# Kernel optimization log

Hardware: AMD Instinct MI355X
Metric: run time of the kernel (lower is better)

The kernel has to match this reference:

```python
import jax, jax.numpy as jnp
import numpy as np

N = 100000   # nodes
E = 1600000  # edges
IN = 3       # in_channels
H = 32       # hidden_channels
C = 10       # num_classes_dynamic (== num output classes here)
G = 64       # number of graphs in the batch


def setup_inputs() -> dict:
    key = jax.random.key(0)
    ks = jax.random.split(key, 12)
    def w(k, shape, fan_in):
        return jax.random.normal(k, shape, jnp.float32) / np.sqrt(fan_in).astype(np.float32)
    inp = {}
    inp["x"] = jax.random.normal(ks[0], (N, IN), jnp.float32)
    inp["edge_index"] = jax.random.randint(ks[1], (2, E), 0, N, jnp.int32)
    inp["batch"] = jnp.sort(jax.random.randint(ks[2], (N,), 0, G, jnp.int32))
    # per-class linear filters (DynamicEdgeConv.filters)
    inp["filt_W"] = w(ks[3], (C, IN, H), IN)
    inp["filt_b"] = jnp.zeros((C, H), jnp.float32)
    # shared edge MLP: Linear(2H,H) -> ReLU -> Linear(H,H)
    inp["mlp_W1"] = w(ks[4], (2 * H, H), 2 * H)
    inp["mlp_b1"] = jnp.zeros((H,), jnp.float32)
    inp["mlp_W2"] = w(ks[5], (H, H), H)
    inp["mlp_b2"] = jnp.zeros((H,), jnp.float32)
    # GCN layers (gcn1 input dim hardcoded 323 = IN + C*H)
    inp["gcn1_W"] = w(ks[6], (IN + C * H, H), IN + C * H)
    inp["gcn1_b"] = jnp.zeros((H,), jnp.float32)
    inp["gcn2_W"] = w(ks[7], (H, H), H)
    inp["gcn2_b"] = jnp.zeros((H,), jnp.float32)
    # classifier
    inp["cls_W"] = w(ks[8], (H, C), H)
    inp["cls_b"] = jnp.zeros((C,), jnp.float32)
    return inp


def _gcn_conv(x, W, b, row, col, dinv):
    # PyG GCNConv: add self-loops, sym-normalize, aggregate src->dst
    xw = x @ W                                   # [N, H]
    norm = dinv[row] * dinv[col]                 # [E]
    out = jax.ops.segment_sum(xw[row] * norm[:, None], col, num_segments=x.shape[0])
    out = out + xw * (dinv * dinv)[:, None]      # self-loop term, norm = 1/deg_i
    return out + b


def _forward(x, edge_index, batch, filt_W, filt_b, mlp_W1, mlp_b1, mlp_W2, mlp_b2,
             gcn1_W, gcn1_b, gcn2_W, gcn2_b, cls_W, cls_b):
    row, col = edge_index[0], edge_index[1]
    n = x.shape[0]

    # DynamicEdgeConv: per-class filter -> gather(row,col) -> edge MLP -> scatter_add into col
    def per_class(_, wb):
        Wc, bc = wb
        xc = x @ Wc + bc                                      # [N, H]
        ef = jnp.concatenate([xc[row], xc[col]], axis=1)      # [E, 2H]
        h = jax.nn.relu(ef @ mlp_W1 + mlp_b1) @ mlp_W2 + mlp_b2
        return None, jax.ops.segment_sum(h, col, num_segments=n)
    _, aggs = jax.lax.scan(per_class, None, (filt_W, filt_b))  # [C, N, H]

    feat = jnp.concatenate([x, aggs.transpose(1, 0, 2).reshape(n, -1)], axis=1)  # [N, IN + C*H]

    deg = jax.ops.segment_sum(jnp.ones(row.shape[0], x.dtype), col, num_segments=n) + 1.0
    dinv = deg ** -0.5
    h1 = jax.nn.relu(_gcn_conv(feat, gcn1_W, gcn1_b, row, col, dinv))
    h2 = jax.nn.relu(_gcn_conv(h1, gcn2_W, gcn2_b, row, col, dinv))

    counts = jax.ops.segment_sum(jnp.ones(n, x.dtype), batch, num_segments=G)
    pooled = jax.ops.segment_sum(h2, batch, num_segments=G) / jnp.maximum(counts, 1.0)[:, None]
    return pooled @ cls_W + cls_b                             # [G, C]


def reference(x, edge_index, batch, filt_W, filt_b, mlp_W1, mlp_b1, mlp_W2, mlp_b2,
              gcn1_W, gcn1_b, gcn2_W, gcn2_b, cls_W, cls_b):
    return _forward(x, edge_index, batch, filt_W, filt_b, mlp_W1, mlp_b1, mlp_W2, mlp_b2,
                    gcn1_W, gcn1_b, gcn2_W, gcn2_b, cls_W, cls_b)
```

## Files before the change

kernel.cpp:

```cpp
#include <hip/hip_runtime.h>

#define NN 100000
#define NE 1600000
#define HH 32
#define CC 10
#define GG 64
#define NB 391
#define PBLK 160
#define ECH 10000
#define MTOT (NB * PBLK)
#define MSB ((MTOT + 255) / 256)

typedef _Float16 half8 __attribute__((ext_vector_type(8)));
typedef _Float16 half2v __attribute__((ext_vector_type(2)));
typedef float f32x4 __attribute__((ext_vector_type(4)));

__device__ __forceinline__ half2v bch(int v) { return __builtin_bit_cast(half2v, v); }


__global__ void precompute_small(const float* __restrict__ fW, const float* __restrict__ fb,
                                 const float* __restrict__ W1, const float* __restrict__ b1,
                                 const float* __restrict__ W2, const float* __restrict__ b2,
                                 const float* __restrict__ g1W, float* __restrict__ tab,
                                 _Float16* __restrict__ Mfrag) {
    int c = blockIdx.x;
    int k = threadIdx.x >> 5;
    int j = threadIdx.x & 31;
    float m = 0.f;
    for (int mm = 0; mm < 32; ++mm)
        m += W2[k * 32 + mm] * g1W[(3 + 32 * c + mm) * 32 + j];
    tab[2240 + c * 1024 + k * 32 + j] = m;

    if (k < 3) {
        float a = 0.f, b = 0.f;
        for (int i = 0; i < 32; ++i) {
            float w = fW[c * 96 + k * 32 + i];
            a += w * W1[i * 32 + j];
            b += w * W1[(32 + i) * 32 + j];
        }
        tab[c * 96 + k * 32 + j] = a;
        tab[960 + c * 96 + k * 32 + j] = b;
    } else if (k == 3) {
        float h = b1[j];
        for (int i = 0; i < 32; ++i)
            h += fb[c * 32 + i] * (W1[i * 32 + j] + W1[(32 + i) * 32 + j]);
        tab[1920 + c * 32 + j] = h;
    } else if (k == 4 && c == 0) {
        float t = 0.f;
        for (int cc2 = 0; cc2 < CC; ++cc2)
            for (int mm = 0; mm < 32; ++mm)
                t += b2[mm] * g1W[(3 + 32 * cc2 + mm) * 32 + j];
        tab[12480 + j] = t;
    }
    __syncthreads();
    {
        int jch = k;
        int jcol = j;
        float v = tab[2240 + c * 1024 + jch * 32 + jcol];
        int knew = (c >> 1) * 64 + 2 * jch + (c & 1);
        int kc = knew >> 5, within = knew & 31;
        int jt = jcol >> 4;
        int lq = within >> 3, ii = within & 7;
        int lidx = lq * 16 + (jcol & 15);
        int flat = ((kc * 2 + jt) * 64 + lidx) * 8 + ii;
        Mfrag[flat] = (_Float16)v;
    }
}

__global__ void bucket_hist(const int* __restrict__ ei, int* __restrict__ mat) {
    __shared__ int h[NB];
    int blk = blockIdx.x, tid = threadIdx.x;
    for (int i = tid; i < NB; i += 256) h[i] = 0;
    __syncthreads();
    int base = blk * ECH;
    for (int k = tid; k < ECH; k += 256)
        atomicAdd(&h[ei[NE + base + k] >> 8], 1);
    __syncthreads();
    for (int i = tid; i < NB; i += 256) mat[i * PBLK + blk] = h[i];
}

__global__ void scan_m1(const int* __restrict__ mat, int* __restrict__ msum) {
    __shared__ int sh[256];
    int b = blockIdx.x, t = threadIdx.x;
    int i = b * 256 + t;
    sh[t] = (i < MTOT) ? mat[i] : 0;
    __syncthreads();
    for (int off = 128; off > 0; off >>= 1) {
        if (t < off) sh[t] += sh[t + off];
        __syncthreads();
    }
    if (t == 0) msum[b] = sh[0];
}

__global__ void scan_m2(int* __restrict__ msum, float* __restrict__ pooled) {
    for (int i = threadIdx.x; i < GG * 33; i += 256) pooled[i] = 0.0f;
    __shared__ int sh[256];
    int t = threadIdx.x;
    int v = (t < MSB) ? msum[t] : 0;
    sh[t] = v;
    __syncthreads();
    for (int off = 1; off < 256; off <<= 1) {
        int add = (t >= off) ? sh[t - off] : 0;
        __syncthreads();
        sh[t] += add;
        __syncthreads();
    }
    if (t < MSB) msum[t] = sh[t] - v;
}

__global__ void scan_m3(int* __restrict__ mat, const int* __restrict__ msum) {
    __shared__ int sh[256];
    int b = blockIdx.x, t = threadIdx.x;
    int i = b * 256 + t;
    int v = (i < MTOT) ? mat[i] : 0;
    sh[t] = v;
    __syncthreads();
    for (int off = 1; off < 256; off <<= 1) {
        int add = (t >= off) ? sh[t - off] : 0;
        __syncthreads();
        sh[t] += add;
        __syncthreads();
    }
    if (i < MTOT) mat[i] = sh[t] - v + msum[b];
}

__global__ void bucket_scatter(const int* __restrict__ ei, const int* __restrict__ mat,
                               unsigned int* __restrict__ part) {
    __shared__ int bas[NB];
    __shared__ int cur[NB];
    int blk = blockIdx.x, tid = threadIdx.x;
    for (int i = tid; i < NB; i += 256) { bas[i] = mat[i * PBLK + blk]; cur[i] = 0; }
    __syncthreads();
    int base = blk * ECH;
    for (int k = tid; k < ECH; k += 256) {
        int e = base + k;
        int r = ei[e];
        int c = ei[NE + e];
        int b = c >> 8;
        int local = atomicAdd(&cur[b], 1);
        part[bas[b] + local] = (unsigned)r | ((unsigned)(c & 255) << 24);
    }
}

__global__ void bucket_build(const unsigned int* __restrict__ part, const int* __restrict__ mat,
                             const float* __restrict__ x, int* __restrict__ csr_row,
                             int* __restrict__ ideg, int* __restrict__ offs,
                             float* __restrict__ dinv, float4* __restrict__ xpad,
                             uint4* __restrict__ xs) {
    __shared__ int lh[256];
    __shared__ int lex[256];
    __shared__ int cur[256];
    int b = blockIdx.x, tid = threadIdx.x;
    int ebase = mat[b * PBLK];
    int eend = (b == NB - 1) ? NE : mat[(b + 1) * PBLK];
    int m = eend - ebase;
    lh[tid] = 0;
    __syncthreads();
    for (int k = tid; k < m; k += 256) {
        unsigned v = part[ebase + k];
        atomicAdd(&lh[v >> 24], 1);
    }
    __syncthreads();
    int cnt = lh[tid];
    lex[tid] = cnt;
    __syncthreads();
    for (int off = 1; off < 256; off <<= 1) {
        int v = (tid >= off) ? lex[tid - off] : 0;
        __syncthreads();
        lex[tid] += v;
        __syncthreads();
    }
    int excl = lex[tid] - cnt;
    lex[tid] = excl;
    cur[tid] = 0;
    int n = b * 256 + tid;
    if (n < NN) {
        ideg[n] = cnt;
        offs[n] = ebase + excl;
        float di = rsqrtf((float)cnt + 1.0f);
        dinv[n] = di;
        float x0 = x[n * 3], x1 = x[n * 3 + 1], x2 = x[n * 3 + 2];
        xpad[n] = make_float4(x0, x1, x2, di);
        _Float16 hx = (_Float16)x0, hy = (_Float16)x1, hz = (_Float16)x2;
        half2v sx = {hx, hx}, sy = {hy, hy}, sz = {hz, hz};
        xs[n] = make_uint4(__builtin_bit_cast(unsigned int, sx),
                           __builtin_bit_cast(unsigned int, sy),
                           __builtin_bit_cast(unsigned int, sz), 0u);
    }
    if (b == 0 && tid == 0) offs[NN] = NE;
    __syncthreads();
    for (int k = tid; k < m; k += 256) {
        unsigned v = part[ebase + k];
        int cl = (int)(v >> 24);
        int r = (int)(v & 0x00FFFFFFu);
        int local = atomicAdd(&cur[cl], 1);
        csr_row[ebase + lex[cl] + local] = r;
    }
}

#define EC_PAIR(QQ, SRC) do { \
    half2v px_ = bch(__shfl((int)(QQ).x, (SRC), 64)); \
    half2v py_ = bch(__shfl((int)(QQ).y, (SRC), 64)); \
    half2v pz_ = bch(__shfl((int)(QQ).z, (SRC), 64)); \
    _Pragma("unroll") \
    for (int p = 0; p < 5; ++p) { \
        half2v v = va[p] + px_ * A0[p] + py_ * A1[p] + pz_ * A2[p]; \
        v = __builtin_elementwise_max(v, zero); \
        acc[p] += v; \
    } } while (0)

#define EC_FLUSH() do { \
    _Pragma("unroll") \
    for (int p = 0; p < 5; ++p) { \
        accf[2 * p]     += (float)acc[p].x; \
        accf[2 * p + 1] += (float)acc[p].y; \
        acc[p] = zero; \
    } } while (0)

#define EC_CHUNK_FROM(T0, QQ, C2) do { \
    int tfull_ = (C2) >> 1; \
    int t_ = (T0); \
    for (; t_ + 4 <= tfull_; t_ += 4) { \
        _Pragma("unroll") \
        for (int u = 0; u < 4; ++u) EC_PAIR(QQ, 2 * (t_ + u) + half); \
        EC_FLUSH(); \
    } \
    for (; t_ < tfull_; ++t_) EC_PAIR(QQ, 2 * t_ + half); \
    if ((C2) & 1) { \
        int src_ = (C2) - 1; \
        half2v px_ = bch(__shfl((int)(QQ).x, src_, 64)); \
        half2v py_ = bch(__shfl((int)(QQ).y, src_, 64)); \
        half2v pz_ = bch(__shfl((int)(QQ).z, src_, 64)); \
        if (half == 0) { \
            _Pragma("unroll") \
            for (int p = 0; p < 5; ++p) { \
                half2v v = va[p] + px_ * A0[p] + py_ * A1[p] + pz_ * A2[p]; \
                v = __builtin_elementwise_max(v, zero); \
                acc[p] += v; \
            } \
        } \
    } \
    EC_FLUSH(); } while (0)

__global__ __launch_bounds__(256, 4) void edgeconv_fused(
    const uint4* __restrict__ xs, const int* __restrict__ offs,
    const int* __restrict__ csr_row, const float* __restrict__ tab,
    _Float16* __restrict__ aggh) {
    int lane = threadIdx.x & 63;
    int j = lane & 31;
    int half = lane >> 5;

    half2v A0[5], A1[5], A2[5], B0[5], B1[5], B2[5], hb[5];
#pragma unroll
    for (int p = 0; p < 5; ++p) {
        int c0 = 2 * p, c1 = 2 * p + 1;
        A0[p] = half2v{(_Float16)tab[c0 * 96 + j],        (_Float16)tab[c1 * 96 + j]};
        A1[p] = half2v{(_Float16)tab[c0 * 96 + 32 + j],   (_Float16)tab[c1 * 96 + 32 + j]};
        A2[p] = half2v{(_Float16)tab[c0 * 96 + 64 + j],   (_Float16)tab[c1 * 96 + 64 + j]};
        B0[p] = half2v{(_Float16)tab[960 + c0 * 96 + j],      (_Float16)tab[960 + c1 * 96 + j]};
        B1[p] = half2v{(_Float16)tab[960 + c0 * 96 + 32 + j], (_Float16)tab[960 + c1 * 96 + 32 + j]};
        B2[p] = half2v{(_Float16)tab[960 + c0 * 96 + 64 + j], (_Float16)tab[960 + c1 * 96 + 64 + j]};
        hb[p] = half2v{(_Float16)tab[1920 + c0 * 32 + j], (_Float16)tab[1920 + c1 * 32 + j]};
    }
    const half2v zero = half2v{(_Float16)0.f, (_Float16)0.f};

    int wid = blockIdx.x * 4 + (threadIdx.x >> 6);
    const int ws = gridDim.x * 4;

    int n = wid;
    if (n >= NN) return;
    int e0 = offs[n];
    int e1 = offs[n + 1];
    uint4 qn = xs[n];
    int n2 = n + ws;
    int e0n = 0, e1n = 0;
    if (n2 < NN) { e0n = offs[n2]; e1n = offs[n2 + 1]; }
    uint4 q;
    {
        int ee = e0 + lane;
        int r0 = (ee < e1) ? csr_row[ee] : 0;
        q = xs[r0];
    }

    while (true) {
        int n3 = n2 + ws;
        int e0n2 = 0, e1n2 = 0;
        if (n3 < NN) { e0n2 = offs[n3]; e1n2 = offs[n3 + 1]; }
        uint4 qn2 = make_uint4(0u, 0u, 0u, 0u);
        if (n2 < NN) qn2 = xs[n2];

        bool multi = (e1 - e0) > 64;
        int pb = multi ? (e0 + 64) : e0n;
        int pe = multi ? e1 : e1n;
        int ee2 = pb + lane;
        int rn = (ee2 < pe) ? csr_row[ee2] : 0;

        half2v pxn = bch((int)qn.x), pyn = bch((int)qn.y), pzn = bch((int)qn.z);
        half2v va[5], acc[5];
        float accf[10];
#pragma unroll
        for (int p = 0; p < 5; ++p) {
            va[p] = hb[p] + pxn * B0[p] + pyn * B1[p] + pzn * B2[p];
            acc[p] = zero;
            accf[2 * p] = 0.f;
            accf[2 * p + 1] = 0.f;
        }

        int c2 = e1 - e0;
        if (c2 > 64) c2 = 64;
        int t0 = 0;
        if ((c2 >> 1) >= 4) {
#pragma unroll
            for (int u = 0; u < 4; ++u) EC_PAIR(q, 2 * u + half);
            EC_FLUSH();
            t0 = 4;
        }
        uint4 qpre = xs[rn];
        EC_CHUNK_FROM(t0, q, c2);

        if (multi) {
            int base = e0 + 64;
            uint4 qc = qpre;
            while (true) {
                int cc = e1 - base;
                if (cc > 64) cc = 64;
                int nb = base + 64;
                bool m2 = nb < e1;
                int pb2 = m2 ? nb : e0n;
                int pe2 = m2 ? e1 : e1n;
                int ee3 = pb2 + lane;
                int rn2 = (ee3 < pe2) ? csr_row[ee3] : 0;
                uint4 qp2 = xs[rn2];
                EC_CHUNK_FROM(0, qc, cc);
                qc = qp2;
                if (!m2) break;
                base = nb;
            }
            qpre = qc;
        }

#pragma unroll
        for (int c = 0; c < 10; ++c) accf[c] += __shfl_xor(accf[c], 32, 64);
        unsigned* arow32 = (unsigned*)(aggh + (size_t)n * 320);
        half2v d0 = {(_Float16)accf[2 * half],     (_Float16)accf[2 * half + 1]};
        half2v d1 = {(_Float16)accf[4 + 2 * half], (_Float16)accf[4 + 2 * half + 1]};
        arow32[lane]      = __builtin_bit_cast(unsigned, d0);
        arow32[64 + lane] = __builtin_bit_cast(unsigned, d1);
        if (half == 0) {
            half2v d2 = {(_Float16)accf[8], (_Float16)accf[9]};
            arow32[128 + lane] = __builtin_bit_cast(unsigned, d2);
        }

        if (n2 >= NN) return;
        n = n2;
        n2 = n3;
        e0 = e0n; e1 = e1n;
        e0n = e0n2; e1n = e1n2;
        qn = qn2;
        q = qpre;
    }
}

__global__ __launch_bounds__(256) void fold_mfma(
    const _Float16* __restrict__ aggh, const _Float16* __restrict__ MfragG,
    const float4* __restrict__ xpad, const int* __restrict__ ideg,
    const float* __restrict__ tab, const float* __restrict__ g1W,
    _Float16* __restrict__ y1) {
    __shared__ _Float16 Mf[10240];
    {
        const uint4* src = (const uint4*)MfragG;
        uint4* dst = (uint4*)Mf;
        for (int i = threadIdx.x; i < 1280; i += 256) dst[i] = src[i];
    }
    __syncthreads();

    int wave = blockIdx.x * 4 + (threadIdx.x >> 6);
    int lane = threadIdx.x & 63;
    int n0 = wave * 16;
    if (n0 >= NN) return;

    int m = lane & 15, q = lane >> 4;
    int arow_n = n0 + m;
    bool rowok = arow_n < NN;
    const _Float16* arow = aggh + (size_t)arow_n * 320 + q * 8;

    const half8* mf = (const half8*)Mf;
    f32x4 acc0 = {0.f, 0.f, 0.f, 0.f};
    f32x4 acc1 = {0.f, 0.f, 0.f, 0.f};

    for (int kc = 0; kc < 10; ++kc) {
        half8 a;
        if (rowok) a = *(const half8*)(arow + kc * 32);
        else {
#pragma unroll
            for (int i = 0; i < 8; ++i) a[i] = (_Float16)0.f;
        }
        half8 b0 = mf[(kc * 2 + 0) * 64 + lane];
        half8 b1 = mf[(kc * 2 + 1) * 64 + lane];
        acc0 = __builtin_amdgcn_mfma_f32_16x16x32_f16(a, b0, acc0, 0, 0, 0);
        acc1 = __builtin_amdgcn_mfma_f32_16x16x32_f16(a, b1, acc1, 0, 0, 0);
    }

    int jcol = lane & 15;
    float t0 = tab[12480 + jcol],      t1 = tab[12480 + 16 + jcol];
    float w00 = g1W[jcol],      w01 = g1W[32 + jcol],      w02 = g1W[64 + jcol];
    float w10 = g1W[16 + jcol], w11 = g1W[48 + jcol],      w12 = g1W[80 + jcol];
#pragma unroll
    for (int r = 0; r < 4; ++r) {
        int node = n0 + q * 4 + r;
        if (node < NN) {
            float4 xn = xpad[node];
            float dg = (float)ideg[node];
            float v0 = dg * t0 + xn.x * w00 + xn.y * w01 + xn.z * w02 + acc0[r];
            float v1 = dg * t1 + xn.x * w10 + xn.y * w11 + xn.z * w12 + acc1[r];
            y1[node * 32 + jcol]      = (_Float16)(v0 * xn.w);
            y1[node * 32 + 16 + jcol] = (_Float16)(v1 * xn.w);
        }
    }
}

__global__ __launch_bounds__(256, 8) void prop1_fused(
    const int* __restrict__ offs, const int* __restrict__ csr_row,
    const unsigned int* __restrict__ y1p, const float* __restrict__ dinv,
    const float* __restrict__ g1b, const float* __restrict__ g2W,
    unsigned int* __restrict__ y2p) {
    __shared__ float g2s[1024];
    for (int i = threadIdx.x; i < 1024; i += 256) g2s[i] = g2W[i];
    __syncthreads();

    int lane = threadIdx.x & 63;
    int l = lane & 15;
    int wid = blockIdx.x * 4 + (threadIdx.x >> 6);
    int n = wid * 4 + (lane >> 4);
    if (n >= NN) return;

    int e0 = offs[n], e1 = offs[n + 1];
    float di = dinv[n];
    half2v pn = __builtin_bit_cast(half2v, y1p[n * 16 + l]);
    float sAl = 0.f, sAh = 0.f, sBl = 0.f, sBh = 0.f;
    int e = e0;
    if (e + 7 < e1) {
        half2v p0[8];
        {
            int r0[8];
#pragma unroll
            for (int u = 0; u < 8; ++u) r0[u] = csr_row[e + u];
#pragma unroll
            for (int u = 0; u < 8; ++u) p0[u] = __builtin_bit_cast(half2v, y1p[r0[u] * 16 + l]);
        }
        while (true) {
            int e2 = e + 8;
            bool more = (e2 + 7 < e1);
            half2v p1[8];
            if (more) {
                int r1[8];
#pragma unroll
                for (int u = 0; u < 8; ++u) r1[u] = csr_row[e2 + u];
#pragma unroll
                for (int u = 0; u < 8; ++u) p1[u] = __builtin_bit_cast(half2v, y1p[r1[u] * 16 + l]);
            }
#pragma unroll
            for (int u = 0; u < 8; u += 2) {
                sAl += (float)p0[u].x;     sAh += (float)p0[u].y;
                sBl += (float)p0[u + 1].x; sBh += (float)p0[u + 1].y;
            }
            e = e2;
            if (!more) break;
#pragma unroll
            for (int u = 0; u < 8; ++u) p0[u] = p1[u];
        }
    }
    if (e + 3 < e1) {
        int r[4];
#pragma unroll
        for (int u = 0; u < 4; ++u) r[u] = csr_row[e + u];
        half2v p[4];
#pragma unroll
        for (int u = 0; u < 4; ++u) p[u] = __builtin_bit_cast(half2v, y1p[r[u] * 16 + l]);
        sAl += (float)p[0].x + (float)p[2].x; sAh += (float)p[0].y + (float)p[2].y;
        sBl += (float)p[1].x + (float)p[3].x; sBh += (float)p[1].y + (float)p[3].y;
        e += 4;
    }
    if (e + 1 < e1) {
        int r0 = csr_row[e], r1 = csr_row[e + 1];
        half2v p0 = __builtin_bit_cast(half2v, y1p[r0 * 16 + l]);
        half2v p1 = __builtin_bit_cast(half2v, y1p[r1 * 16 + l]);
        sAl += (float)p0.x; sAh += (float)p0.y;
        sBl += (float)p1.x; sBh += (float)p1.y;
        e += 2;
    }
    if (e < e1) {
        int r = csr_row[e];
        half2v p = __builtin_bit_cast(half2v, y1p[r * 16 + l]);
        sAl += (float)p.x; sAh += (float)p.y;
    }
    float h1l = di * (sAl + sBl + (float)pn.x);
    float h1h = di * (sAh + sBh + (float)pn.y);
    float hl = fmaxf(h1l + g1b[2 * l], 0.f);
    float hh = fmaxf(h1h + g1b[2 * l + 1], 0.f);

    float al = 0.f, ah = 0.f;
    int base = lane & 48;
#pragma unroll
    for (int m = 0; m < 16; ++m) {
        float xl = __shfl(hl, base + m, 64);
        float xh2 = __shfl(hh, base + m, 64);
        al += xl * g2s[(2 * m) * 32 + 2 * l] + xh2 * g2s[(2 * m + 1) * 32 + 2 * l];
        ah += xl * g2s[(2 * m) * 32 + 2 * l + 1] + xh2 * g2s[(2 * m + 1) * 32 + 2 * l + 1];
    }
    half2v o = {(_Float16)(al * di), (_Float16)(ah * di)};
    y2p[n * 16 + l] = __builtin_bit_cast(unsigned int, o);
}

__global__ __launch_bounds__(256, 8) void prop2_slot(
    const int* __restrict__ offs, const int* __restrict__ csr_row,
    const unsigned int* __restrict__ y2p, const float* __restrict__ dinv,
    unsigned int* __restrict__ outp) {
    int lane = threadIdx.x & 63;
    int l = lane & 15;
    int slot = lane >> 4;
    int n = blockIdx.x * 4 + (threadIdx.x >> 6);
    if (n >= NN) return;

    int e0 = offs[n], e1 = offs[n + 1];
    float di = dinv[n];
    half2v pn = __builtin_bit_cast(half2v, y2p[n * 16 + l]);
    float sl = 0.f, sh = 0.f;
    int e = e0;
    if (e < e1) {
        int i0 = e + slot, i1 = e + 4 + slot;
        int rA = csr_row[(i0 < e1) ? i0 : (e1 - 1)];
        int rB = csr_row[(i1 < e1) ? i1 : (e1 - 1)];
        bool okA = i0 < e1, okB = i1 < e1;
        while (true) {
            half2v pA = __builtin_bit_cast(half2v, y2p[rA * 16 + l]);
            half2v pB = __builtin_bit_cast(half2v, y2p[rB * 16 + l]);
            int en = e + 8;
            bool more = en < e1;
            int rA2 = 0, rB2 = 0;
            bool okA2 = false, okB2 = false;
            if (more) {
                int j0 = en + slot, j1 = en + 4 + slot;
                rA2 = csr_row[(j0 < e1) ? j0 : (e1 - 1)];
                rB2 = csr_row[(j1 < e1) ? j1 : (e1 - 1)];
                okA2 = j0 < e1; okB2 = j1 < e1;
            }
            if (okA) { sl += (float)pA.x; sh += (float)pA.y; }
            if (okB) { sl += (float)pB.x; sh += (float)pB.y; }
            e = en;
            if (!more) break;
            rA = rA2; rB = rB2; okA = okA2; okB = okB2;
        }
    }
    sl += __shfl_xor(sl, 16, 64); sl += __shfl_xor(sl, 32, 64);
    sh += __shfl_xor(sh, 16, 64); sh += __shfl_xor(sh, 32, 64);
    if (slot == 0) {
        half2v o = {(_Float16)(di * (sl + (float)pn.x)),
                    (_Float16)(di * (sh + (float)pn.y))};
        outp[n * 16 + l] = __builtin_bit_cast(unsigned int, o);
    }
}

__global__ void pool_seg(const _Float16* __restrict__ h2, const float* __restrict__ g2b,
                         const int* __restrict__ batch, float* __restrict__ pooled,
                         float* __restrict__ counts) {
    int grp = threadIdx.x >> 5, j = threadIdx.x & 31;
    int base = (blockIdx.x * 8 + grp) * 64;
    if (base >= NN) return;
    float bj = g2b[j];
    float acc = 0.f, cnt = 0.f;
    int curg = -1;
    int lim = base + 64;
    if (lim > NN) lim = NN;
    for (int n = base; n < lim; ++n) {
        int g = batch[n];
        if (g != curg) {
            if (curg >= 0) {
                atomicAdd(&pooled[curg * 32 + j], acc);
                if (j == 0) atomicAdd(&counts[curg], cnt);
            }
            curg = g; acc = 0.f; cnt = 0.f;
        }
        acc += fmaxf((float)h2[n * 32 + j] + bj, 0.f);
        cnt += 1.f;
    }
    if (curg >= 0) {
        atomicAdd(&pooled[curg * 32 + j], acc);
        if (j == 0) atomicAdd(&counts[curg], cnt);
    }
}

__global__ void final_kernel(const float* __restrict__ pooled, const float* __restrict__ counts,
                             const float* __restrict__ clsW, const float* __restrict__ clsb,
                             float* __restrict__ out) {
    int tid = threadIdx.x;
    if (tid >= GG * CC) return;
    int g = tid / CC, cc = tid % CC;
    float inv = 1.0f / fmaxf(counts[g], 1.0f);
    float s = clsb[cc];
    for (int j = 0; j < 32; ++j) s += (pooled[g * 32 + j] * inv) * clsW[j * CC + cc];
    out[g * CC + cc] = s;
}

extern "C" void kernel_launch(void* const* d_in, const int* in_sizes, int n_in,
                              void* d_out, int out_size, void* d_ws, size_t ws_size,
                              hipStream_t stream) {
    const float* x     = (const float*)d_in[0];
    const int*   ei    = (const int*)d_in[1];
    const int*   batch = (const int*)d_in[2];
    const float* fW    = (const float*)d_in[3];
    const float* fb    = (const float*)d_in[4];
    const float* W1    = (const float*)d_in[5];
    const float* b1    = (const float*)d_in[6];
    const float* W2    = (const float*)d_in[7];
    const float* b2    = (const float*)d_in[8];
    const float* g1W   = (const float*)d_in[9];
    const float* g1b   = (const float*)d_in[10];
    const float* g2W   = (const float*)d_in[11];
    const float* g2b   = (const float*)d_in[12];
    const float* clsW  = (const float*)d_in[13];
    const float* clsb  = (const float*)d_in[14];
    float* out = (float*)d_out;

    float4*         xpad    = (float4*)d_ws;
    uint4*          xs      = (uint4*)(xpad + NN);
    _Float16*       aggh    = (_Float16*)(xs + NN);
    unsigned int*   part    = (unsigned int*)aggh;
    int*            csr_row = (int*)(aggh + (size_t)NN * 320);
    int*            mat     = (int*)(csr_row + NE);
    int*            msum    = mat + MTOT;
    int*            ideg    = msum + 256;
    int*            offs    = ideg + NN;
    float*          dinv    = (float*)(offs + NN + 1);
    float*          tab     = dinv + NN;
    _Float16*       Mfrag   = (_Float16*)(tab + 16384);
    _Float16*       y1      = Mfrag + 10240;
    unsigned int*   y2p     = (unsigned int*)(y1 + (size_t)NN * 32);
    unsigned int*   h2p     = y2p + (size_t)NN * 16;
    float*          pooled  = (float*)(h2p + (size_t)NN * 16);
    float*          counts  = pooled + GG * 32;

    const int propBlocks = (NN + 15) / 16;
    const int foldBlocks = ((NN + 15) / 16 + 3) / 4;
    const int slotBlocks = (NN + 3) / 4;

    precompute_small<<<10, 1024, 0, stream>>>(fW, fb, W1, b1, W2, b2, g1W, tab, Mfrag);

    bucket_hist<<<PBLK, 256, 0, stream>>>(ei, mat);
    scan_m1<<<MSB, 256, 0, stream>>>(mat, msum);
    scan_m2<<<1, 256, 0, stream>>>(msum, pooled);
    scan_m3<<<MSB, 256, 0, stream>>>(mat, msum);
    bucket_scatter<<<PBLK, 256, 0, stream>>>(ei, mat, part);
    bucket_build<<<NB, 256, 0, stream>>>(part, mat, x, csr_row, ideg, offs, dinv, xpad, xs);

    edgeconv_fused<<<2048, 256, 0, stream>>>(xs, offs, csr_row, tab, aggh);
    fold_mfma<<<foldBlocks, 256, 0, stream>>>(aggh, Mfrag, xpad, ideg, tab, g1W, y1);

    prop1_fused<<<propBlocks, 256, 0, stream>>>(offs, csr_row, (const unsigned int*)y1,
                                                dinv, g1b, g2W, y2p);
    prop2_slot<<<slotBlocks, 256, 0, stream>>>(offs, csr_row, y2p, dinv, h2p);
    pool_seg<<<(NN + 511) / 512, 256, 0, stream>>>((const _Float16*)h2p, g2b, batch,
                                                   pooled, counts);
    final_kernel<<<1, 640, 0, stream>>>(pooled, counts, clsW, clsb, out);
}
```

Before: 358.6 us.

## Replace two-level bucket sort CSR build with direct atomic degree count and scatter

Replaces the bucketed counting sort (histogram, multi-level scan, bucket scatter, per-bucket local sort) with a global-atomic degree histogram, a scan over node degrees, and a direct atomic scatter of source rows into CSR slots. It also adds nontemporal loads on edge-index and csr_row reads. This removes two passes and the intermediate partition buffer. In exchange it relies on 1.6M global atomics onto random addresses, and the order of neighbors within each row becomes nondeterministic, which can change float summation order.

After: 468.4 us. 30.6% more time.

```diff
diff --git a/kernel.cpp b/kernel.cpp
--- a/kernel.cpp
+++ b/kernel.cpp
@@ -5,11 +5,7 @@
 #define HH 32
 #define CC 10
 #define GG 64
-#define NB 391
-#define PBLK 160
-#define ECH 10000
-#define MTOT (NB * PBLK)
-#define MSB ((MTOT + 255) / 256)
+#define MSB ((NN + 255) / 256)
 
 typedef _Float16 half8 __attribute__((ext_vector_type(8)));
 typedef _Float16 half2v __attribute__((ext_vector_type(2)));
@@ -22,7 +18,11 @@
                                  const float* __restrict__ W1, const float* __restrict__ b1,
                                  const float* __restrict__ W2, const float* __restrict__ b2,
                                  const float* __restrict__ g1W, float* __restrict__ tab,
-                                 _Float16* __restrict__ Mfrag) {
+                                 _Float16* __restrict__ Mfrag,
+                                 int* __restrict__ ideg, int* __restrict__ cnt) {
+    int gid = blockIdx.x * 1024 + threadIdx.x;
+    for (int i = gid; i < NN; i += 10240) { ideg[i] = 0; cnt[i] = 0; }
+
     int c = blockIdx.x;
     int k = threadIdx.x >> 5;
     int j = threadIdx.x & 31;
@@ -67,23 +67,18 @@
     }
 }
 
-__global__ void bucket_hist(const int* __restrict__ ei, int* __restrict__ mat) {
-    __shared__ int h[NB];
-    int blk = blockIdx.x, tid = threadIdx.x;
-    for (int i = tid; i < NB; i += 256) h[i] = 0;
-    __syncthreads();
-    int base = blk * ECH;
-    for (int k = tid; k < ECH; k += 256)
-        atomicAdd(&h[ei[NE + base + k] >> 8], 1);
-    __syncthreads();
-    for (int i = tid; i < NB; i += 256) mat[i * PBLK + blk] = h[i];
-}
-
-__global__ void scan_m1(const int* __restrict__ mat, int* __restrict__ msum) {
+__global__ void deg_hist(const int* __restrict__ ei, int* __restrict__ ideg) {
+    int e = blockIdx.x * 256 + threadIdx.x;
+    if (e >= NE) return;
+    int c = __builtin_nontemporal_load(ei + NE + e);
+    atomicAdd(&ideg[c], 1);
+}
+
+__global__ void scan_m1(const int* __restrict__ deg, int* __restrict__ msum) {
     __shared__ int sh[256];
     int b = blockIdx.x, t = threadIdx.x;
     int i = b * 256 + t;
-    sh[t] = (i < MTOT) ? mat[i] : 0;
+    sh[t] = (i < NN) ? deg[i] : 0;
     __syncthreads();
     for (int off = 128; off > 0; off >>= 1) {
         if (t < off) sh[t] += sh[t + off];
@@ -93,10 +88,29 @@
 }
 
 __global__ void scan_m2(int* __restrict__ msum, float* __restrict__ pooled) {
-    for (int i = threadIdx.x; i < GG * 33; i += 256) pooled[i] = 0.0f;
-    __shared__ int sh[256];
+    for (int i = threadIdx.x; i < GG * 33; i += 512) pooled[i] = 0.0f;
+    __shared__ int sh[512];
     int t = threadIdx.x;
     int v = (t < MSB) ? msum[t] : 0;
+    sh[t] = v;
+    __syncthreads();
+    for (int off = 1; off < 512; off <<= 1) {
+        int add = (t >= off) ? sh[t - off] : 0;
+        __syncthreads();
+        sh[t] += add;
+        __syncthreads();
+    }
+    if (t < MSB) msum[t] = sh[t] - v;
+}
+
+__global__ void scan_m3_init(const int* __restrict__ deg, const int* __restrict__ msum,
+                             const float* __restrict__ x, int* __restrict__ offs,
+                             float* __restrict__ dinv, float4* __restrict__ xpad,
+                             uint4* __restrict__ xs) {
+    __shared__ int sh[256];
+    int b = blockIdx.x, t = threadIdx.x;
+    int i = b * 256 + t;
+    int v = (i < NN) ? deg[i] : 0;
     sh[t] = v;
     __syncthreads();
     for (int off = 1; off < 256; off <<= 1) {
@@ -105,97 +119,29 @@
         sh[t] += add;
         __syncthreads();
     }
-    if (t < MSB) msum[t] = sh[t] - v;
-}
-
-__global__ void scan_m3(int* __restrict__ mat, const int* __restrict__ msum) {
-    __shared__ int sh[256];
-    int b = blockIdx.x, t = threadIdx.x;
-    int i = b * 256 + t;
-    int v = (i < MTOT) ? mat[i] : 0;
-    sh[t] = v;
-    __syncthreads();
-    for (int off = 1; off < 256; off <<= 1) {
-        int add = (t >= off) ? sh[t - off] : 0;
-        __syncthreads();
-        sh[t] += add;
-        __syncthreads();
-    }
-    if (i < MTOT) mat[i] = sh[t] - v + msum[b];
-}
-
-__global__ void bucket_scatter(const int* __restrict__ ei, const int* __restrict__ mat,
-                               unsigned int* __restrict__ part) {
-    __shared__ int bas[NB];
-    __shared__ int cur[NB];
-    int blk = blockIdx.x, tid = threadIdx.x;
-    for (int i = tid; i < NB; i += 256) { bas[i] = mat[i * PBLK + blk]; cur[i] = 0; }
-    __syncthreads();
-    int base = blk * ECH;
-    for (int k = tid; k < ECH; k += 256) {
-        int e = base + k;
-        int r = ei[e];
-        int c = ei[NE + e];
-        int b = c >> 8;
-        int local = atomicAdd(&cur[b], 1);
-        part[bas[b] + local] = (unsigned)r | ((unsigned)(c & 255) << 24);
-    }
-}
-
-__global__ void bucket_build(const unsigned int* __restrict__ part, const int* __restrict__ mat,
-                             const float* __restrict__ x, int* __restrict__ csr_row,
-                             int* __restrict__ ideg, int* __restrict__ offs,
-                             float* __restrict__ dinv, float4* __restrict__ xpad,
-                             uint4* __restrict__ xs) {
-    __shared__ int lh[256];
-    __shared__ int lex[256];
-    __shared__ int cur[256];
-    int b = blockIdx.x, tid = threadIdx.x;
-    int ebase = mat[b * PBLK];
-    int eend = (b == NB - 1) ? NE : mat[(b + 1) * PBLK];
-    int m = eend - ebase;
-    lh[tid] = 0;
-    __syncthreads();
-    for (int k = tid; k < m; k += 256) {
-        unsigned v = part[ebase + k];
-        atomicAdd(&lh[v >> 24], 1);
-    }
-    __syncthreads();
-    int cnt = lh[tid];
-    lex[tid] = cnt;
-    __syncthreads();
-    for (int off = 1; off < 256; off <<= 1) {
-        int v = (tid >= off) ? lex[tid - off] : 0;
-        __syncthreads();
-        lex[tid] += v;
-        __syncthreads();
-    }
-    int excl = lex[tid] - cnt;
-    lex[tid] = excl;
-    cur[tid] = 0;
-    int n = b * 256 + tid;
-    if (n < NN) {
-        ideg[n] = cnt;
-        offs[n] = ebase + excl;
-        float di = rsqrtf((float)cnt + 1.0f);
-        dinv[n] = di;
-        float x0 = x[n * 3], x1 = x[n * 3 + 1], x2 = x[n * 3 + 2];
-        xpad[n] = make_float4(x0, x1, x2, di);
+    if (i < NN) {
+        offs[i] = sh[t] - v + msum[b];
+        float di = rsqrtf((float)v + 1.0f);
+        dinv[i] = di;
+        float x0 = x[i * 3], x1 = x[i * 3 + 1], x2 = x[i * 3 + 2];
+        xpad[i] = make_float4(x0, x1, x2, di);
         _Float16 hx = (_Float16)x0, hy = (_Float16)x1, hz = (_Float16)x2;
         half2v sx = {hx, hx}, sy = {hy, hy}, sz = {hz, hz};
-        xs[n] = make_uint4(__builtin_bit_cast(unsigned int, sx),
+        xs[i] = make_uint4(__builtin_bit_cast(unsigned int, sx),
                            __builtin_bit_cast(unsigned int, sy),
                            __builtin_bit_cast(unsigned int, sz), 0u);
     }
-    if (b == 0 && tid == 0) offs[NN] = NE;
-    __syncthreads();
-    for (int k = tid; k < m; k += 256) {
-        unsigned v = part[ebase + k];
-        int cl = (int)(v >> 24);
-        int r = (int)(v & 0x00FFFFFFu);
-        int local = atomicAdd(&cur[cl], 1);
-        csr_row[ebase + lex[cl] + local] = r;
-    }
+    if (b == 0 && t == 0) offs[NN] = NE;
+}
+
+__global__ void scatter_direct(const int* __restrict__ ei, const int* __restrict__ offs,
+                               int* __restrict__ cnt, int* __restrict__ csr_row) {
+    int e = blockIdx.x * 256 + threadIdx.x;
+    if (e >= NE) return;
+    int r = __builtin_nontemporal_load(ei + e);
+    int c = __builtin_nontemporal_load(ei + NE + e);
+    int local = atomicAdd(&cnt[c], 1);
+    csr_row[offs[c] + local] = r;
 }
 
 #define EC_PAIR(QQ, SRC) do { \
@@ -278,7 +224,7 @@
     uint4 q;
     {
         int ee = e0 + lane;
-        int r0 = (ee < e1) ? csr_row[ee] : 0;
+        int r0 = (ee < e1) ? __builtin_nontemporal_load(csr_row + ee) : 0;
         q = xs[r0];
     }
 
@@ -293,7 +239,7 @@
         int pb = multi ? (e0 + 64) : e0n;
         int pe = multi ? e1 : e1n;
         int ee2 = pb + lane;
-        int rn = (ee2 < pe) ? csr_row[ee2] : 0;
+        int rn = (ee2 < pe) ? __builtin_nontemporal_load(csr_row + ee2) : 0;
 
         half2v pxn = bch((int)qn.x), pyn = bch((int)qn.y), pzn = bch((int)qn.z);
         half2v va[5], acc[5];
@@ -329,7 +275,7 @@
                 int pb2 = m2 ? nb : e0n;
                 int pe2 = m2 ? e1 : e1n;
                 int ee3 = pb2 + lane;
-                int rn2 = (ee3 < pe2) ? csr_row[ee3] : 0;
+                int rn2 = (ee3 < pe2) ? __builtin_nontemporal_load(csr_row + ee3) : 0;
                 uint4 qp2 = xs[rn2];
                 EC_CHUNK_FROM(0, qc, cc);
                 qc = qp2;
@@ -625,11 +571,10 @@
     float4*         xpad    = (float4*)d_ws;
     uint4*          xs      = (uint4*)(xpad + NN);
     _Float16*       aggh    = (_Float16*)(xs + NN);
-    unsigned int*   part    = (unsigned int*)aggh;
     int*            csr_row = (int*)(aggh + (size_t)NN * 320);
-    int*            mat     = (int*)(csr_row + NE);
-    int*            msum    = mat + MTOT;
-    int*            ideg    = msum + 256;
+    int*            cnt     = csr_row + NE;
+    int*            msum    = cnt + NN;
+    int*            ideg    = msum + 512;
     int*            offs    = ideg + NN;
     float*          dinv    = (float*)(offs + NN + 1);
     float*          tab     = dinv + NN;
@@ -643,15 +588,15 @@
     const int propBlocks = (NN + 15) / 16;
     const int foldBlocks = ((NN + 15) / 16 + 3) / 4;
     const int slotBlocks = (NN + 3) / 4;
-
-    precompute_small<<<10, 1024, 0, stream>>>(fW, fb, W1, b1, W2, b2, g1W, tab, Mfrag);
-
-    bucket_hist<<<PBLK, 256, 0, stream>>>(ei, mat);
-    scan_m1<<<MSB, 256, 0, stream>>>(mat, msum);
-    scan_m2<<<1, 256, 0, stream>>>(msum, pooled);
-    scan_m3<<<MSB, 256, 0, stream>>>(mat, msum);
-    bucket_scatter<<<PBLK, 256, 0, stream>>>(ei, mat, part);
-    bucket_build<<<NB, 256, 0, stream>>>(part, mat, x, csr_row, ideg, offs, dinv, xpad, xs);
+    const int edgeBlocks = (NE + 255) / 256;
+
+    precompute_small<<<10, 1024, 0, stream>>>(fW, fb, W1, b1, W2, b2, g1W, tab, Mfrag,
+                                              ideg, cnt);
+    deg_hist<<<edgeBlocks, 256, 0, stream>>>(ei, ideg);
+    scan_m1<<<MSB, 256, 0, stream>>>(ideg, msum);
+    scan_m2<<<1, 512, 0, stream>>>(msum, pooled);
+    scan_m3_init<<<MSB, 256, 0, stream>>>(ideg, msum, x, offs, dinv, xpad, xs);
+    scatter_direct<<<edgeBlocks, 256, 0, stream>>>(ei, offs, cnt, csr_row);
 
     edgeconv_fused<<<2048, 256, 0, stream>>>(xs, offs, csr_row, tab, aggh);
     fold_mfma<<<foldBlocks, 256, 0, stream>>>(aggh, Mfrag, xpad, ideg, tab, g1W, y1);
```
